# Kernel optimization log

Measured on AMD Instinct MI355X. Metric: run time of the kernel, lower is better.

Reference implementation:

```python
import jax, jax.numpy as jnp
import numpy as np

E = 1024      # embedding_size
H = 16        # num_head
DQ = DK = DV = 64  # per-head q/k/v size


def setup_inputs() -> dict:
    key = jax.random.key(0)
    ks = jax.random.split(key, 9)
    B, S = 2, 2048
    s = 1.0 / np.sqrt(E)
    return {
        "q": jax.random.normal(ks[0], (B, S, E), jnp.float32),
        "k": jax.random.normal(ks[1], (B, S, E), jnp.float32),
        "v": jax.random.normal(ks[2], (B, S, E), jnp.float32),
        "w_q": jax.random.normal(ks[3], (E, H * DQ), jnp.float32) * s,
        "b_q": jax.random.normal(ks[4], (H * DQ,), jnp.float32) * s,
        "w_k": jax.random.normal(ks[5], (E, H * DK), jnp.float32) * s,
        "b_k": jax.random.normal(ks[6], (H * DK,), jnp.float32) * s,
        "w_v": jax.random.normal(ks[7], (E, H * DV), jnp.float32) * s,
        "b_v": jax.random.normal(ks[8], (H * DV,), jnp.float32) * s,
    }


def reference(q, k, v, w_q, b_q, w_k, b_k, w_v, b_v):
    B, Sq, _ = q.shape
    Sk = k.shape[1]
    # projections -> [B, S, H, d] -> [B, H, S, d]
    qh = (q @ w_q + b_q).reshape(B, Sq, H, DQ).transpose(0, 2, 1, 3)
    kh = (k @ w_k + b_k).reshape(B, Sk, H, DK).transpose(0, 2, 1, 3)
    vh = (v @ w_v + b_v).reshape(B, Sk, H, DV).transpose(0, 2, 1, 3)
    # scaled dot-product attention; scores [B, H, Sq, Sk]
    scores = jnp.einsum("bhqd,bhkd->bhqk", qh, kh) / jnp.sqrt(jnp.float32(DQ))
    weights = jax.nn.softmax(scores, axis=-1)
    out = jnp.einsum("bhqk,bhkd->bhqd", weights, vh)  # [B, H, Sq, DV]
    return out.transpose(0, 2, 1, 3).reshape(B, Sq, H * DV)
```

## Files before the change

kernel.cpp:

```cpp
#include <hip/hip_runtime.h>
#include <hip/hip_bf16.h>

typedef __bf16 bf16_t;
typedef bf16_t bf16x8 __attribute__((ext_vector_type(8)));
typedef bf16_t bf16x4 __attribute__((ext_vector_type(4)));
typedef short  short4v __attribute__((ext_vector_type(4)));
typedef float  f32x4  __attribute__((ext_vector_type(4)));

#define MFMA16(a,b,c) __builtin_amdgcn_mfma_f32_16x16x32_bf16(a, b, c, 0, 0, 0)

static __device__ inline f32x4 mfma_k16(bf16x4 a, bf16x4 b, f32x4 c) {
#if __has_builtin(__builtin_amdgcn_mfma_f32_16x16x16_bf16)
  return __builtin_amdgcn_mfma_f32_16x16x16_bf16(a, b, c, 0, 0, 0);
#else
  return __builtin_amdgcn_mfma_f32_16x16x16bf16_1k(
      __builtin_bit_cast(short4v, a), __builtin_bit_cast(short4v, b), c, 0, 0, 0);
#endif
}

constexpr int S = 2048, H = 16, Dh = 64;
constexpr int N = H * Dh;
constexpr int K = 1024;
constexpr float QSCALE = 0.125f * 1.4426950408889634f;

static __device__ inline void load_lds16(const bf16_t* g, bf16_t* l) {
  __builtin_amdgcn_global_load_lds(
      (const __attribute__((address_space(1))) void*)g,
      (__attribute__((address_space(3))) void*)l, 16, 0, 0);
}

static __device__ inline ushort f2bb(float x) {
  bf16_t h = (bf16_t)x;
  return __builtin_bit_cast(ushort, h);
}

__global__ __launch_bounds__(256) void prep(
    const float* __restrict__ q, const float* __restrict__ k,
    const float* __restrict__ v,
    const float* __restrict__ wq, const float* __restrict__ wk,
    const float* __restrict__ wv,
    bf16_t* __restrict__ xq, bf16_t* __restrict__ xk, bf16_t* __restrict__ xv,
    bf16_t* __restrict__ wtq, bf16_t* __restrict__ wtk, bf16_t* __restrict__ wtv) {
  __shared__ ushort tile[64][68];
  int bx = blockIdx.x, t = threadIdx.x;
  if (bx < 6144) {
    int z = bx >> 11, bb = bx & 2047;
    const float* xi = z == 0 ? q : z == 1 ? k : v;
    bf16_t*      xo = z == 0 ? xq : z == 1 ? xk : xv;
    size_t idx = ((size_t)bb * 256 + t) * 8;
    float4 a = *(const float4*)&xi[idx];
    float4 b = *(const float4*)&xi[idx + 4];
    bf16x8 w;
    w[0] = (bf16_t)a.x; w[1] = (bf16_t)a.y; w[2] = (bf16_t)a.z; w[3] = (bf16_t)a.w;
    w[4] = (bf16_t)b.x; w[5] = (bf16_t)b.y; w[6] = (bf16_t)b.z; w[7] = (bf16_t)b.w;
    *(bf16x8*)&xo[idx] = w;
  } else {
    int zz = bx - 6144;
    int z = zz >> 8, bb = zz & 255;
    const float* wi = z == 0 ? wq : z == 1 ? wk : wv;
    ushort*      wo = (ushort*)(z == 0 ? wtq : z == 1 ? wtk : wtv);
    int k0 = (bb >> 4) * 64, n0 = (bb & 15) * 64;
    for (int i = 0; i < 4; ++i) {
      int idx4 = (i * 256 + t) * 4;
      int r = idx4 >> 6, c = idx4 & 63;
      float4 vv = *(const float4*)&wi[(size_t)(k0 + r) * N + n0 + c];
      tile[r][c] = f2bb(vv.x); tile[r][c + 1] = f2bb(vv.y);
      tile[r][c + 2] = f2bb(vv.z); tile[r][c + 3] = f2bb(vv.w);
    }
    __syncthreads();
    for (int i = 0; i < 4; ++i) {
      int idx4 = (i * 256 + t) * 4;
      int r = idx4 >> 6, c = idx4 & 63;
      ushort4 vv;
      vv.x = tile[c][r]; vv.y = tile[c + 1][r];
      vv.z = tile[c + 2][r]; vv.w = tile[c + 3][r];
      *(ushort4*)&wo[(size_t)(n0 + r) * K + k0 + c] = vv;
    }
  }
}

__global__ __launch_bounds__(256) void proj_gemm(
    const bf16_t* __restrict__ xq, const bf16_t* __restrict__ xk,
    const bf16_t* __restrict__ xv,
    const bf16_t* __restrict__ wtq, const bf16_t* __restrict__ wtk,
    const bf16_t* __restrict__ wtv,
    const float* __restrict__ bq, const float* __restrict__ bk,
    const float* __restrict__ bv,
    bf16_t* __restrict__ qh, bf16_t* __restrict__ kh, bf16_t* __restrict__ vt) {
  int mode = blockIdx.z;
  const bf16_t* X  = mode == 0 ? xq  : mode == 1 ? xk  : wtv;
  const bf16_t* Wt = mode == 0 ? wtq : mode == 1 ? wtk : xv;
  const float*  Bi = mode == 0 ? bq  : mode == 1 ? bk  : bv;

  __shared__ bf16_t smem[17408];
  bf16_t (*Ash)[64] = (bf16_t(*)[64])smem;
  bf16_t (*Bsh)[64] = (bf16_t(*)[64])(smem + 8192);
  bf16_t* Cs = smem;

  int tid = threadIdx.x;
  int wave = tid >> 6, lane = tid & 63;
  int lr = lane & 15, lg = lane >> 4;
  int lrow = lane >> 3, lchunk = lane & 7;
  int m0 = (mode < 2 ? blockIdx.y : blockIdx.x) * 128;
  int n0 = (mode < 2 ? blockIdx.x : blockIdx.y) * 128;
  int wm = (wave >> 1) * 64, wn = (wave & 1) * 64;

  f32x4 acc[4][4];
  for (int i = 0; i < 4; ++i)
    for (int j = 0; j < 4; ++j) acc[i][j] = (f32x4){0.f, 0.f, 0.f, 0.f};

  for (int ko = 0; ko < K / 64; ++ko) {
    __syncthreads();
    for (int j = 0; j < 4; ++j) {
      int r = wave * 32 + j * 8 + lrow;
      int gc = (lchunk ^ (r & 7)) * 8;
      load_lds16(&X [(size_t)(m0 + r) * K + ko * 64 + gc], &Ash[r][lchunk * 8]);
      load_lds16(&Wt[(size_t)(n0 + r) * K + ko * 64 + gc], &Bsh[r][lchunk * 8]);
    }
    __syncthreads();
    for (int kk = 0; kk < 2; ++kk) {
      bf16x8 af[4], bfr[4];
      for (int i = 0; i < 4; ++i) {
        int rr = wm + i * 16 + lr;
        af[i] = *(const bf16x8*)&Ash[rr][(((kk << 2) | lg) ^ (rr & 7)) * 8];
      }
      for (int j = 0; j < 4; ++j) {
        int rr = wn + j * 16 + lr;
        bfr[j] = *(const bf16x8*)&Bsh[rr][(((kk << 2) | lg) ^ (rr & 7)) * 8];
      }
      for (int i = 0; i < 4; ++i)
        for (int j = 0; j < 4; ++j)
          acc[i][j] = MFMA16(af[i], bfr[j], acc[i][j]);
    }
  }

  float badd[4][4][4];
  if (mode < 2) {
    float bvv[4];
    for (int j = 0; j < 4; ++j) bvv[j] = Bi[n0 + wn + j * 16 + lr];
    for (int i = 0; i < 4; ++i)
      for (int j = 0; j < 4; ++j)
        for (int r = 0; r < 4; ++r) badd[i][j][r] = bvv[j];
  } else {
    for (int i = 0; i < 4; ++i)
      for (int r = 0; r < 4; ++r) {
        float bm = Bi[m0 + wm + i * 16 + lg * 4 + r];
        for (int j = 0; j < 4; ++j) badd[i][j][r] = bm;
      }
  }

  __syncthreads();
  for (int i = 0; i < 4; ++i)
    for (int j = 0; j < 4; ++j)
      for (int r = 0; r < 4; ++r) {
        float vvv = acc[i][j][r] + badd[i][j][r];
        if (mode == 0) vvv *= QSCALE;
        Cs[(size_t)(wm + i * 16 + lg * 4 + r) * 136 + wn + j * 16 + lr] = (bf16_t)vvv;
      }
  __syncthreads();

  bf16_t* o = mode == 0 ? qh : mode == 1 ? kh : vt;
  for (int p = 0; p < 8; ++p) {
    int idx = p * 256 + tid;
    int row = idx >> 4, ch = idx & 15;
    bf16x8 vv = *(const bf16x8*)&Cs[(size_t)row * 136 + ch * 8];
    size_t dst;
    if (mode < 2) {
      int m_g = m0 + row;
      int n_g = n0 + ch * 8;
      int b = m_g >> 11, s = m_g & 2047;
      int h = n_g >> 6, d = n_g & 63;
      dst = (((size_t)(b * 16 + h) * 2048) + s) * 64 + d;
    } else {
      int w_g = m0 + row;
      int t_g = n0 + ch * 8;
      int b = t_g >> 11, s = t_g & 2047;
      dst = ((size_t)(b * 1024 + w_g)) * 2048 + s;
    }
    *(uint4*)&o[dst] = __builtin_bit_cast(uint4, vv);
  }
}

__global__ __launch_bounds__(256) void attn(
    const bf16_t* __restrict__ qh, const bf16_t* __restrict__ kh,
    const bf16_t* __restrict__ vt, float* __restrict__ out) {
  __shared__ bf16_t kt[64][64];
  __shared__ bf16_t vs[64][64];

  int tid = threadIdx.x, wave = tid >> 6, lane = tid & 63;
  int lr = lane & 15, lg = lane >> 4;
  int lrow = lane >> 3, lchunk = lane & 7;
  int bh = blockIdx.y;
  int q0 = blockIdx.x * 128 + wave * 32;

  const bf16_t* qg = qh + (size_t)bh * S * Dh;
  const bf16_t* kg = kh + (size_t)bh * S * Dh;
  const bf16_t* vg = vt + (size_t)bh * Dh * S;

  bf16x8 bq[2][2];
  for (int ms = 0; ms < 2; ++ms)
    for (int kk = 0; kk < 2; ++kk)
      bq[ms][kk] = *(const bf16x8*)&qg[(size_t)(q0 + ms * 16 + lr) * 64 + kk * 32 + lg * 8];

  bf16x4 ones;
  ones[0] = (bf16_t)1.0f; ones[1] = (bf16_t)1.0f;
  ones[2] = (bf16_t)1.0f; ones[3] = (bf16_t)1.0f;

  f32x4 o_acc[2][4], lacc[2];
  for (int ms = 0; ms < 2; ++ms) {
    lacc[ms] = (f32x4){0.f, 0.f, 0.f, 0.f};
    for (int t = 0; t < 4; ++t) o_acc[ms][t] = (f32x4){0.f, 0.f, 0.f, 0.f};
  }

  for (int it = 0; it < S / 64; ++it) {
    int sk0 = it * 64;
    __syncthreads();
    for (int j = 0; j < 2; ++j) {
      int r = wave * 16 + j * 8 + lrow;
      int gc = (lchunk ^ (r & 7)) * 8;
      load_lds16(&kg[(size_t)(sk0 + r) * 64 + gc], &kt[r][lchunk * 8]);
      load_lds16(&vg[(size_t)r * S + sk0 + gc], &vs[r][lchunk * 8]);
    }
    __syncthreads();

    bf16x8 ak[4][2];
    for (int t = 0; t < 4; ++t)
      for (int kk = 0; kk < 2; ++kk)
        ak[t][kk] = *(const bf16x8*)&kt[t * 16 + lr][((kk * 4 + lg) ^ (lr & 7)) * 8];
    bf16x4 bv[4][4];
    for (int t = 0; t < 4; ++t)
      for (int dt = 0; dt < 4; ++dt)
        bv[t][dt] = *(const bf16x4*)
            &vs[dt * 16 + lr][(((t * 2 + (lg >> 1)) ^ (lr & 7)) * 8) + (lg & 1) * 4];

    for (int ms = 0; ms < 2; ++ms) {
      f32x4 st[4];
      for (int t = 0; t < 4; ++t) st[t] = (f32x4){0.f, 0.f, 0.f, 0.f};
      for (int t = 0; t < 4; ++t)
        for (int kk = 0; kk < 2; ++kk)
          st[t] = MFMA16(ak[t][kk], bq[ms][kk], st[t]);

      bf16x4 pa[4];
      for (int t = 0; t < 4; ++t)
        for (int r = 0; r < 4; ++r)
          pa[t][r] = (bf16_t)__builtin_amdgcn_exp2f(st[t][r]);

      for (int t = 0; t < 4; ++t) {
        for (int dt = 0; dt < 4; ++dt)
          o_acc[ms][dt] = mfma_k16(pa[t], bv[t][dt], o_acc[ms][dt]);
        lacc[ms] = mfma_k16(pa[t], ones, lacc[ms]);
      }
    }
  }

  int b = bh >> 4, h = bh & 15;
  for (int ms = 0; ms < 2; ++ms)
    for (int r = 0; r < 4; ++r) {
      float inv = 1.f / lacc[ms][r];
      int s_row = q0 + ms * 16 + lg * 4 + r;
      size_t base = ((size_t)(b * S + s_row)) * 1024 + h * 64;
      for (int dt = 0; dt < 4; ++dt)
        out[base + dt * 16 + lr] = o_acc[ms][dt][r] * inv;
    }
}

extern "C" void kernel_launch(void* const* d_in, const int* in_sizes, int n_in,
                              void* d_out, int out_size, void* d_ws, size_t ws_size,
                              hipStream_t stream) {
  const float* q  = (const float*)d_in[0];
  const float* k  = (const float*)d_in[1];
  const float* v  = (const float*)d_in[2];
  const float* wq = (const float*)d_in[3];
  const float* bq = (const float*)d_in[4];
  const float* wk = (const float*)d_in[5];
  const float* bk = (const float*)d_in[6];
  const float* wv = (const float*)d_in[7];
  const float* bv = (const float*)d_in[8];

  bf16_t* ws  = (bf16_t*)d_ws;
  constexpr size_t MW = (size_t)1 << 20;
  constexpr size_t MX = (size_t)4096 * 1024;
  bf16_t* wtq = ws;
  bf16_t* wtk = wtq + MW;
  bf16_t* wtv = wtk + MW;
  bf16_t* xq  = wtv + MW;
  bf16_t* xk  = xq + MX;
  bf16_t* xv  = xk + MX;
  bf16_t* qhd = xv + MX;
  bf16_t* khd = qhd + MX;
  bf16_t* vtd = khd + MX;
  float* out  = (float*)d_out;

  prep<<<6912, 256, 0, stream>>>(q, k, v, wq, wk, wv,
                                 xq, xk, xv, wtq, wtk, wtv);
  proj_gemm<<<dim3(8, 32, 3), 256, 0, stream>>>(xq, xk, xv, wtq, wtk, wtv,
                                                bq, bk, bv, qhd, khd, vtd);
  attn<<<dim3(16, 32), 256, 0, stream>>>(qhd, khd, vtd, out);
}
```

Baseline: 208.4 us.

## Fuse prep, projection GEMM and attention into one persistent kernel with grid barriers

Replaces the three launches (conversion/transpose prep, projection GEMM, attention) with a single persistent kernel of 768 blocks. The phases are separated by software grid barriers built on atomic counters in workspace. The goal is to remove kernel launch overhead and the tail drain between stages. In exchange, all 768 blocks must be co-resident, which is why launch bounds are set to 3 blocks per CU. The barrier reset also depends on the workspace counter starting at a 0xAAAAAAAA fill pattern, so repeated calls without that fill could race.

Measured after the change: 678.1 us. 3.25x slower.

```diff
diff --git a/kernel.cpp b/kernel.cpp
--- a/kernel.cpp
+++ b/kernel.cpp
@@ -21,6 +21,7 @@
 constexpr int S = 2048, H = 16, Dh = 64;
 constexpr int N = H * Dh;
 constexpr int K = 1024;
+constexpr int GRID = 768;
 constexpr float QSCALE = 0.125f * 1.4426950408889634f;
 
 static __device__ inline void load_lds16(const bf16_t* g, bf16_t* l) {
@@ -34,34 +35,57 @@
   return __builtin_bit_cast(ushort, h);
 }
 
-__global__ __launch_bounds__(256) void prep(
+static __device__ inline void grid_barrier(unsigned* C, int tid) {
+  __threadfence();
+  __syncthreads();
+  if (tid == 0) {
+    atomicCAS(C, 0xAAAAAAAAu, 0u);
+    atomicAdd(C, 1u);
+    while (__hip_atomic_load(C, __ATOMIC_ACQUIRE, __HIP_MEMORY_SCOPE_AGENT) < GRID)
+      __builtin_amdgcn_s_sleep(1);
+  }
+  __syncthreads();
+  __threadfence();
+}
+
+__global__ __launch_bounds__(256, 3) void fused(
     const float* __restrict__ q, const float* __restrict__ k,
     const float* __restrict__ v,
     const float* __restrict__ wq, const float* __restrict__ wk,
     const float* __restrict__ wv,
+    const float* __restrict__ bq, const float* __restrict__ bk,
+    const float* __restrict__ bv,
     bf16_t* __restrict__ xq, bf16_t* __restrict__ xk, bf16_t* __restrict__ xv,
-    bf16_t* __restrict__ wtq, bf16_t* __restrict__ wtk, bf16_t* __restrict__ wtv) {
-  __shared__ ushort tile[64][68];
-  int bx = blockIdx.x, t = threadIdx.x;
-  if (bx < 6144) {
-    int z = bx >> 11, bb = bx & 2047;
+    bf16_t* __restrict__ wtq, bf16_t* __restrict__ wtk, bf16_t* __restrict__ wtv,
+    bf16_t* __restrict__ qh, bf16_t* __restrict__ kh, bf16_t* __restrict__ vt,
+    unsigned* __restrict__ bar, float* __restrict__ out) {
+  __shared__ __align__(16) bf16_t smem[17408];
+
+  int bid = blockIdx.x, tid = threadIdx.x;
+  int wave = tid >> 6, lane = tid & 63;
+  int lr = lane & 15, lg = lane >> 4;
+  int lrow = lane >> 3, lchunk = lane & 7;
+
+  {
+    int z = bid >> 8, bb = bid & 255;
     const float* xi = z == 0 ? q : z == 1 ? k : v;
     bf16_t*      xo = z == 0 ? xq : z == 1 ? xk : xv;
-    size_t idx = ((size_t)bb * 256 + t) * 8;
-    float4 a = *(const float4*)&xi[idx];
-    float4 b = *(const float4*)&xi[idx + 4];
-    bf16x8 w;
-    w[0] = (bf16_t)a.x; w[1] = (bf16_t)a.y; w[2] = (bf16_t)a.z; w[3] = (bf16_t)a.w;
-    w[4] = (bf16_t)b.x; w[5] = (bf16_t)b.y; w[6] = (bf16_t)b.z; w[7] = (bf16_t)b.w;
-    *(bf16x8*)&xo[idx] = w;
-  } else {
-    int zz = bx - 6144;
-    int z = zz >> 8, bb = zz & 255;
+    size_t base = (size_t)bb * 16384;
+    for (int i = 0; i < 8; ++i) {
+      size_t idx = base + (size_t)i * 2048 + tid * 8;
+      float4 a = *(const float4*)&xi[idx];
+      float4 b = *(const float4*)&xi[idx + 4];
+      bf16x8 w;
+      w[0] = (bf16_t)a.x; w[1] = (bf16_t)a.y; w[2] = (bf16_t)a.z; w[3] = (bf16_t)a.w;
+      w[4] = (bf16_t)b.x; w[5] = (bf16_t)b.y; w[6] = (bf16_t)b.z; w[7] = (bf16_t)b.w;
+      *(bf16x8*)&xo[idx] = w;
+    }
+    ushort (*tile)[68] = (ushort(*)[68])smem;
     const float* wi = z == 0 ? wq : z == 1 ? wk : wv;
     ushort*      wo = (ushort*)(z == 0 ? wtq : z == 1 ? wtk : wtv);
     int k0 = (bb >> 4) * 64, n0 = (bb & 15) * 64;
     for (int i = 0; i < 4; ++i) {
-      int idx4 = (i * 256 + t) * 4;
+      int idx4 = (i * 256 + tid) * 4;
       int r = idx4 >> 6, c = idx4 & 63;
       float4 vv = *(const float4*)&wi[(size_t)(k0 + r) * N + n0 + c];
       tile[r][c] = f2bb(vv.x); tile[r][c + 1] = f2bb(vv.y);
@@ -69,7 +93,7 @@
     }
     __syncthreads();
     for (int i = 0; i < 4; ++i) {
-      int idx4 = (i * 256 + t) * 4;
+      int idx4 = (i * 256 + tid) * 4;
       int r = idx4 >> 6, c = idx4 & 63;
       ushort4 vv;
       vv.x = tile[c][r]; vv.y = tile[c + 1][r];
@@ -77,191 +101,182 @@
       *(ushort4*)&wo[(size_t)(n0 + r) * K + k0 + c] = vv;
     }
   }
-}
-
-__global__ __launch_bounds__(256) void proj_gemm(
-    const bf16_t* __restrict__ xq, const bf16_t* __restrict__ xk,
-    const bf16_t* __restrict__ xv,
-    const bf16_t* __restrict__ wtq, const bf16_t* __restrict__ wtk,
-    const bf16_t* __restrict__ wtv,
-    const float* __restrict__ bq, const float* __restrict__ bk,
-    const float* __restrict__ bv,
-    bf16_t* __restrict__ qh, bf16_t* __restrict__ kh, bf16_t* __restrict__ vt) {
-  int mode = blockIdx.z;
-  const bf16_t* X  = mode == 0 ? xq  : mode == 1 ? xk  : wtv;
-  const bf16_t* Wt = mode == 0 ? wtq : mode == 1 ? wtk : xv;
-  const float*  Bi = mode == 0 ? bq  : mode == 1 ? bk  : bv;
-
-  __shared__ bf16_t smem[17408];
-  bf16_t (*Ash)[64] = (bf16_t(*)[64])smem;
-  bf16_t (*Bsh)[64] = (bf16_t(*)[64])(smem + 8192);
-  bf16_t* Cs = smem;
-
-  int tid = threadIdx.x;
-  int wave = tid >> 6, lane = tid & 63;
-  int lr = lane & 15, lg = lane >> 4;
-  int lrow = lane >> 3, lchunk = lane & 7;
-  int m0 = (mode < 2 ? blockIdx.y : blockIdx.x) * 128;
-  int n0 = (mode < 2 ? blockIdx.x : blockIdx.y) * 128;
-  int wm = (wave >> 1) * 64, wn = (wave & 1) * 64;
-
-  f32x4 acc[4][4];
-  for (int i = 0; i < 4; ++i)
-    for (int j = 0; j < 4; ++j) acc[i][j] = (f32x4){0.f, 0.f, 0.f, 0.f};
-
-  for (int ko = 0; ko < K / 64; ++ko) {
-    __syncthreads();
-    for (int j = 0; j < 4; ++j) {
-      int r = wave * 32 + j * 8 + lrow;
-      int gc = (lchunk ^ (r & 7)) * 8;
-      load_lds16(&X [(size_t)(m0 + r) * K + ko * 64 + gc], &Ash[r][lchunk * 8]);
-      load_lds16(&Wt[(size_t)(n0 + r) * K + ko * 64 + gc], &Bsh[r][lchunk * 8]);
-    }
-    __syncthreads();
-    for (int kk = 0; kk < 2; ++kk) {
-      bf16x8 af[4], bfr[4];
-      for (int i = 0; i < 4; ++i) {
-        int rr = wm + i * 16 + lr;
-        af[i] = *(const bf16x8*)&Ash[rr][(((kk << 2) | lg) ^ (rr & 7)) * 8];
-      }
+
+  grid_barrier(bar, tid);
+
+  {
+    int mode = bid >> 8, r8 = bid & 255;
+    int by = r8 >> 3, bx = r8 & 7;
+    const bf16_t* X  = mode == 0 ? xq  : mode == 1 ? xk  : wtv;
+    const bf16_t* Wt = mode == 0 ? wtq : mode == 1 ? wtk : xv;
+    const float*  Bi = mode == 0 ? bq  : mode == 1 ? bk  : bv;
+
+    bf16_t (*Ash)[64] = (bf16_t(*)[64])smem;
+    bf16_t (*Bsh)[64] = (bf16_t(*)[64])(smem + 8192);
+    bf16_t* Cs = smem;
+
+    int m0 = (mode < 2 ? by : bx) * 128;
+    int n0 = (mode < 2 ? bx : by) * 128;
+    int wm = (wave >> 1) * 64, wn = (wave & 1) * 64;
+
+    f32x4 acc[4][4];
+    for (int i = 0; i < 4; ++i)
+      for (int j = 0; j < 4; ++j) acc[i][j] = (f32x4){0.f, 0.f, 0.f, 0.f};
+
+    for (int ko = 0; ko < K / 64; ++ko) {
+      __syncthreads();
       for (int j = 0; j < 4; ++j) {
-        int rr = wn + j * 16 + lr;
-        bfr[j] = *(const bf16x8*)&Bsh[rr][(((kk << 2) | lg) ^ (rr & 7)) * 8];
-      }
+        int r = wave * 32 + j * 8 + lrow;
+        int gc = (lchunk ^ (r & 7)) * 8;
+        load_lds16(&X [(size_t)(m0 + r) * K + ko * 64 + gc], &Ash[r][lchunk * 8]);
+        load_lds16(&Wt[(size_t)(n0 + r) * K + ko * 64 + gc], &Bsh[r][lchunk * 8]);
+      }
+      __syncthreads();
+      for (int kk = 0; kk < 2; ++kk) {
+        bf16x8 af[4], bfr[4];
+        for (int i = 0; i < 4; ++i) {
+          int rr = wm + i * 16 + lr;
+          af[i] = *(const bf16x8*)&Ash[rr][(((kk << 2) | lg) ^ (rr & 7)) * 8];
+        }
+        for (int j = 0; j < 4; ++j) {
+          int rr = wn + j * 16 + lr;
+          bfr[j] = *(const bf16x8*)&Bsh[rr][(((kk << 2) | lg) ^ (rr & 7)) * 8];
+        }
+        for (int i = 0; i < 4; ++i)
+          for (int j = 0; j < 4; ++j)
+            acc[i][j] = MFMA16(af[i], bfr[j], acc[i][j]);
+      }
+    }
+
+    float badd[4][4][4];
+    if (mode < 2) {
+      float bvv[4];
+      for (int j = 0; j < 4; ++j) bvv[j] = Bi[n0 + wn + j * 16 + lr];
       for (int i = 0; i < 4; ++i)
         for (int j = 0; j < 4; ++j)
-          acc[i][j] = MFMA16(af[i], bfr[j], acc[i][j]);
-    }
-  }
-
-  float badd[4][4][4];
-  if (mode < 2) {
-    float bvv[4];
-    for (int j = 0; j < 4; ++j) bvv[j] = Bi[n0 + wn + j * 16 + lr];
+          for (int r = 0; r < 4; ++r) badd[i][j][r] = bvv[j];
+    } else {
+      for (int i = 0; i < 4; ++i)
+        for (int r = 0; r < 4; ++r) {
+          float bm = Bi[m0 + wm + i * 16 + lg * 4 + r];
+          for (int j = 0; j < 4; ++j) badd[i][j][r] = bm;
+        }
+    }
+
+    __syncthreads();
     for (int i = 0; i < 4; ++i)
       for (int j = 0; j < 4; ++j)
-        for (int r = 0; r < 4; ++r) badd[i][j][r] = bvv[j];
-  } else {
-    for (int i = 0; i < 4; ++i)
-      for (int r = 0; r < 4; ++r) {
-        float bm = Bi[m0 + wm + i * 16 + lg * 4 + r];
-        for (int j = 0; j < 4; ++j) badd[i][j][r] = bm;
-      }
+        for (int r = 0; r < 4; ++r) {
+          float vvv = acc[i][j][r] + badd[i][j][r];
+          if (mode == 0) vvv *= QSCALE;
+          Cs[(size_t)(wm + i * 16 + lg * 4 + r) * 136 + wn + j * 16 + lr] = (bf16_t)vvv;
+        }
+    __syncthreads();
+
+    bf16_t* o = mode == 0 ? qh : mode == 1 ? kh : vt;
+    for (int p = 0; p < 8; ++p) {
+      int idx = p * 256 + tid;
+      int row = idx >> 4, ch = idx & 15;
+      bf16x8 vv = *(const bf16x8*)&Cs[(size_t)row * 136 + ch * 8];
+      size_t dst;
+      if (mode < 2) {
+        int m_g = m0 + row, n_g = n0 + ch * 8;
+        int b = m_g >> 11, s = m_g & 2047;
+        int h = n_g >> 6, d = n_g & 63;
+        dst = (((size_t)(b * 16 + h) * 2048) + s) * 64 + d;
+      } else {
+        int w_g = m0 + row, t_g = n0 + ch * 8;
+        int b = t_g >> 11, s = t_g & 2047;
+        dst = ((size_t)(b * 1024 + w_g)) * 2048 + s;
+      }
+      *(uint4*)&o[dst] = __builtin_bit_cast(uint4, vv);
+    }
   }
 
-  __syncthreads();
-  for (int i = 0; i < 4; ++i)
-    for (int j = 0; j < 4; ++j)
-      for (int r = 0; r < 4; ++r) {
-        float vvv = acc[i][j][r] + badd[i][j][r];
-        if (mode == 0) vvv *= QSCALE;
-        Cs[(size_t)(wm + i * 16 + lg * 4 + r) * 136 + wn + j * 16 + lr] = (bf16_t)vvv;
-      }
-  __syncthreads();
-
-  bf16_t* o = mode == 0 ? qh : mode == 1 ? kh : vt;
-  for (int p = 0; p < 8; ++p) {
-    int idx = p * 256 + tid;
-    int row = idx >> 4, ch = idx & 15;
-    bf16x8 vv = *(const bf16x8*)&Cs[(size_t)row * 136 + ch * 8];
-    size_t dst;
-    if (mode < 2) {
-      int m_g = m0 + row;
-      int n_g = n0 + ch * 8;
-      int b = m_g >> 11, s = m_g & 2047;
-      int h = n_g >> 6, d = n_g & 63;
-      dst = (((size_t)(b * 16 + h) * 2048) + s) * 64 + d;
-    } else {
-      int w_g = m0 + row;
-      int t_g = n0 + ch * 8;
-      int b = t_g >> 11, s = t_g & 2047;
-      dst = ((size_t)(b * 1024 + w_g)) * 2048 + s;
-    }
-    *(uint4*)&o[dst] = __builtin_bit_cast(uint4, vv);
-  }
-}
-
-__global__ __launch_bounds__(256) void attn(
-    const bf16_t* __restrict__ qh, const bf16_t* __restrict__ kh,
-    const bf16_t* __restrict__ vt, float* __restrict__ out) {
-  __shared__ bf16_t kt[64][64];
-  __shared__ bf16_t vs[64][64];
-
-  int tid = threadIdx.x, wave = tid >> 6, lane = tid & 63;
-  int lr = lane & 15, lg = lane >> 4;
-  int lrow = lane >> 3, lchunk = lane & 7;
-  int bh = blockIdx.y;
-  int q0 = blockIdx.x * 128 + wave * 32;
-
-  const bf16_t* qg = qh + (size_t)bh * S * Dh;
-  const bf16_t* kg = kh + (size_t)bh * S * Dh;
-  const bf16_t* vg = vt + (size_t)bh * Dh * S;
-
-  bf16x8 bq[2][2];
-  for (int ms = 0; ms < 2; ++ms)
+  grid_barrier(bar + 64, tid);
+
+  if (bid < 512) {
+    bf16_t (*kt)[64] = (bf16_t(*)[64])smem;
+    bf16_t (*vs)[64] = (bf16_t(*)[64])(smem + 4096);
+
+    int bh = bid >> 4;
+    int q0 = (bid & 15) * 128 + wave * 32;
+
+    const bf16_t* qg = qh + (size_t)bh * S * Dh;
+    const bf16_t* kg = kh + (size_t)bh * S * Dh;
+    const bf16_t* vg = vt + (size_t)bh * Dh * S;
+
+    bf16x8 bqf[2][2];
+    for (int ms = 0; ms < 2; ++ms)
+      for (int kk = 0; kk < 2; ++kk)
+        bqf[ms][kk] = *(const bf16x8*)&qg[(size_t)(q0 + ms * 16 + lr) * 64 + kk * 32 + lg * 8];
+
+    bf16x4 ones;
+    ones[0] = (bf16_t)1.0f; ones[1] = (bf16_t)1.0f;
+    ones[2] = (bf16_t)1.0f; ones[3] = (bf16_t)1.0f;
+
+    f32x4 o_acc[2][4], lacc[2];
+    for (int ms = 0; ms < 2; ++ms) {
+      lacc[ms] = (f32x4){0.f, 0.f, 0.f, 0.f};
+      for (int t = 0; t < 4; ++t) o_acc[ms][t] = (f32x4){0.f, 0.f, 0.f, 0.f};
+    }
+
+    int akoff[2], bvoff[4];
     for (int kk = 0; kk < 2; ++kk)
-      bq[ms][kk] = *(const bf16x8*)&qg[(size_t)(q0 + ms * 16 + lr) * 64 + kk * 32 + lg * 8];
-
-  bf16x4 ones;
-  ones[0] = (bf16_t)1.0f; ones[1] = (bf16_t)1.0f;
-  ones[2] = (bf16_t)1.0f; ones[3] = (bf16_t)1.0f;
-
-  f32x4 o_acc[2][4], lacc[2];
-  for (int ms = 0; ms < 2; ++ms) {
-    lacc[ms] = (f32x4){0.f, 0.f, 0.f, 0.f};
-    for (int t = 0; t < 4; ++t) o_acc[ms][t] = (f32x4){0.f, 0.f, 0.f, 0.f};
-  }
-
-  for (int it = 0; it < S / 64; ++it) {
-    int sk0 = it * 64;
-    __syncthreads();
-    for (int j = 0; j < 2; ++j) {
-      int r = wave * 16 + j * 8 + lrow;
-      int gc = (lchunk ^ (r & 7)) * 8;
-      load_lds16(&kg[(size_t)(sk0 + r) * 64 + gc], &kt[r][lchunk * 8]);
-      load_lds16(&vg[(size_t)r * S + sk0 + gc], &vs[r][lchunk * 8]);
-    }
-    __syncthreads();
-
-    bf16x8 ak[4][2];
+      akoff[kk] = lr * 64 + (((kk << 2) | lg) ^ (lr & 7)) * 8;
     for (int t = 0; t < 4; ++t)
-      for (int kk = 0; kk < 2; ++kk)
-        ak[t][kk] = *(const bf16x8*)&kt[t * 16 + lr][((kk * 4 + lg) ^ (lr & 7)) * 8];
-    bf16x4 bv[4][4];
-    for (int t = 0; t < 4; ++t)
-      for (int dt = 0; dt < 4; ++dt)
-        bv[t][dt] = *(const bf16x4*)
-            &vs[dt * 16 + lr][(((t * 2 + (lg >> 1)) ^ (lr & 7)) * 8) + (lg & 1) * 4];
-
-    for (int ms = 0; ms < 2; ++ms) {
-      f32x4 st[4];
-      for (int t = 0; t < 4; ++t) st[t] = (f32x4){0.f, 0.f, 0.f, 0.f};
+      bvoff[t] = lr * 64 + (((t * 2 + (lg >> 1)) ^ (lr & 7)) * 8) + (lg & 1) * 4;
+
+    for (int it = 0; it < S / 64; ++it) {
+      int sk0 = it * 64;
+      __syncthreads();
+      for (int j = 0; j < 2; ++j) {
+        int r = wave * 16 + j * 8 + lrow;
+        int gc = (lchunk ^ (r & 7)) * 8;
+        load_lds16(&kg[(size_t)(sk0 + r) * 64 + gc], &kt[r][lchunk * 8]);
+        load_lds16(&vg[(size_t)r * S + sk0 + gc], &vs[r][lchunk * 8]);
+      }
+      __syncthreads();
+
+      bf16x8 ak[4][2];
       for (int t = 0; t < 4; ++t)
         for (int kk = 0; kk < 2; ++kk)
-          st[t] = MFMA16(ak[t][kk], bq[ms][kk], st[t]);
-
-      bf16x4 pa[4];
+          ak[t][kk] = *(const bf16x8*)&((bf16_t*)kt)[t * 1024 + akoff[kk]];
+      bf16x4 bv[4][4];
       for (int t = 0; t < 4; ++t)
-        for (int r = 0; r < 4; ++r)
-          pa[t][r] = (bf16_t)__builtin_amdgcn_exp2f(st[t][r]);
-
-      for (int t = 0; t < 4; ++t) {
         for (int dt = 0; dt < 4; ++dt)
-          o_acc[ms][dt] = mfma_k16(pa[t], bv[t][dt], o_acc[ms][dt]);
-        lacc[ms] = mfma_k16(pa[t], ones, lacc[ms]);
-      }
-    }
+          bv[t][dt] = *(const bf16x4*)&((bf16_t*)vs)[dt * 1024 + bvoff[t]];
+
+      for (int ms = 0; ms < 2; ++ms) {
+        f32x4 st[4];
+        for (int t = 0; t < 4; ++t) st[t] = (f32x4){0.f, 0.f, 0.f, 0.f};
+        for (int t = 0; t < 4; ++t)
+          for (int kk = 0; kk < 2; ++kk)
+            st[t] = MFMA16(ak[t][kk], bqf[ms][kk], st[t]);
+
+        bf16x4 pa[4];
+        for (int t = 0; t < 4; ++t)
+          for (int r = 0; r < 4; ++r)
+            pa[t][r] = (bf16_t)__builtin_amdgcn_exp2f(st[t][r]);
+
+        for (int t = 0; t < 4; ++t) {
+          for (int dt = 0; dt < 4; ++dt)
+            o_acc[ms][dt] = mfma_k16(pa[t], bv[t][dt], o_acc[ms][dt]);
+          lacc[ms] = mfma_k16(pa[t], ones, lacc[ms]);
+        }
+      }
+    }
+
+    int b = bh >> 4, h = bh & 15;
+    for (int ms = 0; ms < 2; ++ms)
+      for (int r = 0; r < 4; ++r) {
+        float inv = 1.f / lacc[ms][r];
+        int s_row = q0 + ms * 16 + lg * 4 + r;
+        size_t base = ((size_t)(b * S + s_row)) * 1024 + h * 64;
+        for (int dt = 0; dt < 4; ++dt)
+          out[base + dt * 16 + lr] = o_acc[ms][dt][r] * inv;
+      }
   }
-
-  int b = bh >> 4, h = bh & 15;
-  for (int ms = 0; ms < 2; ++ms)
-    for (int r = 0; r < 4; ++r) {
-      float inv = 1.f / lacc[ms][r];
-      int s_row = q0 + ms * 16 + lg * 4 + r;
-      size_t base = ((size_t)(b * S + s_row)) * 1024 + h * 64;
-      for (int dt = 0; dt < 4; ++dt)
-        out[base + dt * 16 + lr] = o_acc[ms][dt][r] * inv;
-    }
 }
 
 extern "C" void kernel_launch(void* const* d_in, const int* in_sizes, int n_in,
@@ -289,11 +304,10 @@
   bf16_t* qhd = xv + MX;
   bf16_t* khd = qhd + MX;
   bf16_t* vtd = khd + MX;
+  unsigned* bar = (unsigned*)(vtd + MX);
   float* out  = (float*)d_out;
 
-  prep<<<6912, 256, 0, stream>>>(q, k, v, wq, wk, wv,
-                                 xq, xk, xv, wtq, wtk, wtv);
-  proj_gemm<<<dim3(8, 32, 3), 256, 0, stream>>>(xq, xk, xv, wtq, wtk, wtv,
-                                                bq, bk, bv, qhd, khd, vtd);
-  attn<<<dim3(16, 32), 256, 0, stream>>>(qhd, khd, vtd, out);
-}
+  fused<<<GRID, 256, 0, stream>>>(q, k, v, wq, wk, wv, bq, bk, bv,
+                                  xq, xk, xv, wtq, wtk, wtv,
+                                  qhd, khd, vtd, bar, out);
+}
```
